# Kernel optimization log

Measured on AMD Instinct MI355X. Metric: run time of the kernel, lower is better.

## Reference

```python
import jax, jax.numpy as jnp
import numpy as np

I, H = 4, 64


def setup_inputs() -> dict:
    key = jax.random.key(0)
    ks = jax.random.split(key, 7)
    s_ih = 1.0 / np.sqrt(H)
    return {
        "x": jax.random.normal(ks[0], (8192, 512, I), dtype=jnp.float32),
        "W_ih": jax.random.uniform(ks[1], (4 * H, I), minval=-s_ih, maxval=s_ih, dtype=jnp.float32),
        "W_hh": jax.random.uniform(ks[2], (4 * H, H), minval=-s_ih, maxval=s_ih, dtype=jnp.float32),
        "b_ih": jax.random.uniform(ks[3], (4 * H,), minval=-s_ih, maxval=s_ih, dtype=jnp.float32),
        "b_hh": jax.random.uniform(ks[4], (4 * H,), minval=-s_ih, maxval=s_ih, dtype=jnp.float32),
        "W_fc": jax.random.uniform(ks[5], (1, H), minval=-s_ih, maxval=s_ih, dtype=jnp.float32),
        "b_fc": jax.random.uniform(ks[6], (1,), minval=-s_ih, maxval=s_ih, dtype=jnp.float32),
    }


def _lstm_last_hidden(x, W_ih, W_hh, b_ih, b_hh):
    # x: [B, T, I] batch_first; PyTorch gate order: i, f, g, o
    B = x.shape[0]
    # Precompute input projections for all timesteps in one GEMM: [T, B, 4H]
    xg = jnp.einsum('bti,gi->tbg', x, W_ih) + (b_ih + b_hh)

    def step(carry, xg_t):
        h, c = carry
        gates = xg_t + h @ W_hh.T  # [B, 4H]
        i, f, g, o = jnp.split(gates, 4, axis=-1)
        i = jax.nn.sigmoid(i)
        f = jax.nn.sigmoid(f)
        g = jnp.tanh(g)
        o = jax.nn.sigmoid(o)
        c = f * c + i * g
        h = o * jnp.tanh(c)
        return (h, c), None

    h0 = jnp.zeros((B, W_hh.shape[1]), dtype=x.dtype)
    c0 = jnp.zeros_like(h0)
    (h_n, _), _ = jax.lax.scan(step, (h0, c0), xg)
    return h_n  # [B, H]


def reference(x, W_ih, W_hh, b_ih, b_hh, W_fc, b_fc):
    h_n = _lstm_last_hidden(x, W_ih, W_hh, b_ih, b_hh)
    return h_n @ W_fc.T + b_fc  # [B, 1]
```

## Files before the change

### kernel.cpp

```cpp
#include <hip/hip_runtime.h>


typedef float f32x4 __attribute__((ext_vector_type(4)));
typedef _Float16 f16x8 __attribute__((ext_vector_type(8)));
typedef _Float16 f16x4 __attribute__((ext_vector_type(4)));

#define TSEQ 512
#define IDIM 4
#define BPB 16
#define TCH 32
#define NCH (TSEQ / TCH)
#define L2E 1.44269504088896340736f

#if __has_builtin(__builtin_amdgcn_exp2f)
#define EX2(v) __builtin_amdgcn_exp2f(v)
#else
#define EX2(v) exp2f(v)
#endif
#define RCP(v) __builtin_amdgcn_rcpf(v)

#define STEP_BARRIER() do {                                   \
    asm volatile("s_waitcnt lgkmcnt(0)" ::: "memory");        \
    __builtin_amdgcn_s_barrier();                             \
    __builtin_amdgcn_sched_barrier(0);                        \
} while (0)

__global__ __launch_bounds__(256, 2) void lstm_fused(
    const float* __restrict__ x,
    const float* __restrict__ W_ih,
    const float* __restrict__ W_hh,
    const float* __restrict__ b_ih,
    const float* __restrict__ b_hh,
    const float* __restrict__ W_fc,
    const float* __restrict__ b_fc,
    float* __restrict__ out)
{
    __shared__ __align__(16) _Float16 hbuf[2][BPB * 64];
    __shared__ __align__(16) f16x4    xstage[2][BPB][33];

    const int tid  = threadIdx.x;
    const int lane = tid & 63;
    const int wv   = tid >> 6;
    const int b0   = blockIdx.x * BPB;
    const int r    = lane & 15;
    const int g16  = lane >> 4;

    f16x8 bfrag[4][3];
    #pragma unroll
    for (int t4 = 0; t4 < 4; ++t4) {
        const float sc = (t4 == 2) ? 2.0f * L2E : L2E;
        const int g = t4 * 64 + wv * 16 + r;
        #pragma unroll
        for (int ks = 0; ks < 2; ++ks) {
            const float* p = W_hh + g * 64 + ks * 32 + g16 * 8;
            f16x8 f;
            #pragma unroll
            for (int j = 0; j < 8; ++j) f[j] = (_Float16)(p[j] * sc);
            bfrag[t4][ks] = f;
        }
        f16x8 f;
        #pragma unroll
        for (int j = 0; j < 8; ++j) f[j] = (_Float16)0.0f;
        if (g16 == 0) {
            #pragma unroll
            for (int j = 0; j < 4; ++j) f[j] = (_Float16)(W_ih[g * IDIM + j] * sc);
            float biasf = (b_ih[g] + b_hh[g]) * sc;
            _Float16 hi = (_Float16)biasf;
            f[4] = hi;
            f[5] = (_Float16)(biasf - (float)hi);
        }
        bfrag[t4][2] = f;
    }
    const float wfc = W_fc[lane];
    const float bfc = b_fc[0];
    const f32x4 zero4 = {0.f, 0.f, 0.f, 0.f};

    float c_reg[4] = {0.f, 0.f, 0.f, 0.f};
    for (int i = tid; i < BPB * 64; i += 256) hbuf[0][i] = (_Float16)0.0f;

    const int bb0 = tid >> 5, tf = tid & 31;
    const float* xg0 = x + ((size_t)(b0 + bb0)     * TSEQ + tf) * IDIM;
    const float* xg1 = x + ((size_t)(b0 + bb0 + 8) * TSEQ + tf) * IDIM;
    float4 xn0 = *(const float4*)xg0;
    float4 xn1 = *(const float4*)xg1;
    {
        f16x4 s0, s1;
        s0[0] = (_Float16)xn0.x; s0[1] = (_Float16)xn0.y;
        s0[2] = (_Float16)xn0.z; s0[3] = (_Float16)xn0.w;
        s1[0] = (_Float16)xn1.x; s1[1] = (_Float16)xn1.y;
        s1[2] = (_Float16)xn1.z; s1[3] = (_Float16)xn1.w;
        xstage[0][bb0][tf]     = s0;
        xstage[0][bb0 + 8][tf] = s1;
    }
    __syncthreads();
    xn0 = *(const float4*)(xg0 + TCH * IDIM);
    xn1 = *(const float4*)(xg1 + TCH * IDIM);

    const int hbase = r * 128;
    const int hs0 = ((g16 + 0) << 4) ^ ((r & 7) << 4);
    const int hs1 = ((g16 + 4) << 4) ^ ((r & 7) << 4);
    int hw[4];
    #pragma unroll
    for (int q = 0; q < 4; ++q) {
        const int bat = 4 * g16 + q;
        hw[q] = (bat * 128 + (wv * 16 + r) * 2) ^ ((bat & 7) << 4);
    }
    char* hbB = (char*)&hbuf[0][0];
    const char* xsB = (const char*)&xstage[0][0][0];
    const int xrow = r * 33 * 8;

    f16x8 axr;
    axr[4] = (_Float16)1.0f; axr[5] = (_Float16)1.0f;
    axr[6] = (_Float16)0.0f; axr[7] = (_Float16)0.0f;

    f32x4 accX[4];
    {
        f16x4 xv = *(const f16x4*)(xsB + xrow);
        axr[0] = xv[0]; axr[1] = xv[1]; axr[2] = xv[2]; axr[3] = xv[3];
        #pragma unroll
        for (int t4 = 0; t4 < 4; ++t4)
            accX[t4] = __builtin_amdgcn_mfma_f32_16x16x32_f16(axr, bfrag[t4][2], zero4, 0, 0, 0);
    }

    auto substep = [&](int t, int P) {
        const char* rb = hbB + P * 2048;
        char*       wb = hbB + (P ^ 1) * 2048;
        f16x8 a0 = *(const f16x8*)(rb + hbase + hs0);
        f16x8 a1 = *(const f16x8*)(rb + hbase + hs1);

        f32x4 acc2[4];
        __builtin_amdgcn_s_setprio(1);
        #pragma unroll
        for (int t4 = 0; t4 < 4; ++t4) {
            f32x4 a;
            a = __builtin_amdgcn_mfma_f32_16x16x32_f16(a0, bfrag[t4][0], accX[t4], 0, 0, 0);
            a = __builtin_amdgcn_mfma_f32_16x16x32_f16(a1, bfrag[t4][1], a, 0, 0, 0);
            acc2[t4] = a;
        }
        __builtin_amdgcn_s_setprio(0);

        {
            const int tb = t + 1;
            f16x4 xv = *(const f16x4*)(xsB + ((tb >> 5) & 1) * 4224 + xrow + (tb & 31) * 8);
            axr[0] = xv[0]; axr[1] = xv[1]; axr[2] = xv[2]; axr[3] = xv[3];
            __builtin_amdgcn_s_setprio(1);
            #pragma unroll
            for (int t4 = 0; t4 < 4; ++t4)
                accX[t4] = __builtin_amdgcn_mfma_f32_16x16x32_f16(axr, bfrag[t4][2], zero4, 0, 0, 0);
            __builtin_amdgcn_s_setprio(0);
        }

        #pragma unroll
        for (int q = 0; q < 4; ++q) {
            float ei = EX2(-acc2[0][q]);
            float ef = EX2(-acc2[1][q]);
            float eg = EX2(-acc2[2][q]);
            float eo = EX2(-acc2[3][q]);
            float A  = 1.f + ei, F = 1.f + ef;
            float Gp = 1.f + eg, Gm = 1.f - eg;
            float P2  = A * Gp;
            float num = c_reg[q] * P2 + Gm * F;
            float c   = num * RCP(P2 * F);
            c_reg[q] = c;
            float uc = fminf(fmaxf(c * (2.0f * L2E), -60.f), 60.f);
            float et = EX2(-uc);
            float h  = (1.f - et) * RCP((1.f + eo) * (1.f + et));
            *(_Float16*)(wb + hw[q]) = (_Float16)h;
        }
        STEP_BARRIER();
    };

    for (int t = 0; t < TSEQ; t += 2) {
        if ((t & (TCH - 1)) == 16) {
            const int c = t >> 5;
            if (c + 1 < NCH) {
                f16x4 s0, s1;
                s0[0] = (_Float16)xn0.x; s0[1] = (_Float16)xn0.y;
                s0[2] = (_Float16)xn0.z; s0[3] = (_Float16)xn0.w;
                s1[0] = (_Float16)xn1.x; s1[1] = (_Float16)xn1.y;
                s1[2] = (_Float16)xn1.z; s1[3] = (_Float16)xn1.w;
                f16x4* dst = &xstage[(c + 1) & 1][0][0];
                dst[bb0 * 33 + tf]       = s0;
                dst[(bb0 + 8) * 33 + tf] = s1;
                if (c + 2 < NCH) {
                    xn0 = *(const float4*)(xg0 + (size_t)(c + 2) * TCH * IDIM);
                    xn1 = *(const float4*)(xg1 + (size_t)(c + 2) * TCH * IDIM);
                }
            }
        }
        substep(t,     0);
        substep(t + 1, 1);
    }

    #pragma unroll
    for (int q = 0; q < 4; ++q) {
        const int bat  = wv * 4 + q;
        const int byte = (bat * 128 + lane * 2) ^ ((bat & 7) << 4);
        float hv = (float)*(const _Float16*)(hbB + byte);
        float partial = hv * wfc;
        #pragma unroll
        for (int off = 32; off > 0; off >>= 1)
            partial += __shfl_down(partial, off);
        if (lane == 0) out[b0 + bat] = partial + bfc;
    }
}

extern "C" void kernel_launch(void* const* d_in, const int* in_sizes, int n_in,
                              void* d_out, int out_size, void* d_ws, size_t ws_size,
                              hipStream_t stream) {
    const float* x    = (const float*)d_in[0];
    const float* W_ih = (const float*)d_in[1];
    const float* W_hh = (const float*)d_in[2];
    const float* b_ih = (const float*)d_in[3];
    const float* b_hh = (const float*)d_in[4];
    const float* W_fc = (const float*)d_in[5];
    const float* b_fc = (const float*)d_in[6];
    float* out = (float*)d_out;

    const int B = in_sizes[0] / (TSEQ * IDIM);
    lstm_fused<<<B / BPB, 256, 0, stream>>>(x, W_ih, W_hh, b_ih, b_hh, W_fc, b_fc, out);
}
```

Before: 338.7 us.

## Inline input-projection MFMA into recurrent chain and stagger alternate blocks

Removes the software-pipelined precomputation of the input projection for the next step and instead chains a third MFMA (x·W_ih plus bias) after the two recurrent MFMAs, starting from zero. It also drops the sched_barrier from the step barrier so the compiler can reorder across steps. Odd blocks (by a simple blockIdx hash) sleep briefly at start to desynchronise co-resident blocks so their MFMA and transcendental phases interleave. The cost is a longer dependent MFMA chain on the critical path per step.

```diff
diff --git a/kernel.cpp b/kernel.cpp
--- a/kernel.cpp
+++ b/kernel.cpp
@@ -22,7 +22,6 @@
 #define STEP_BARRIER() do {                                   \
     asm volatile("s_waitcnt lgkmcnt(0)" ::: "memory");        \
     __builtin_amdgcn_s_barrier();                             \
-    __builtin_amdgcn_sched_barrier(0);                        \
 } while (0)
 
 __global__ __launch_bounds__(256, 2) void lstm_fused(
@@ -96,6 +95,9 @@
     xn0 = *(const float4*)(xg0 + TCH * IDIM);
     xn1 = *(const float4*)(xg1 + TCH * IDIM);
 
+    if (((blockIdx.x ^ (blockIdx.x >> 8)) & 1) != 0)
+        __builtin_amdgcn_s_sleep(13);
+
     const int hbase = r * 128;
     const int hs0 = ((g16 + 0) << 4) ^ ((r & 7) << 4);
     const int hs1 = ((g16 + 4) << 4) ^ ((r & 7) << 4);
@@ -109,53 +111,35 @@
     const char* xsB = (const char*)&xstage[0][0][0];
     const int xrow = r * 33 * 8;
 
-    f16x8 axr;
-    axr[4] = (_Float16)1.0f; axr[5] = (_Float16)1.0f;
-    axr[6] = (_Float16)0.0f; axr[7] = (_Float16)0.0f;
-
-    f32x4 accX[4];
-    {
-        f16x4 xv = *(const f16x4*)(xsB + xrow);
-        axr[0] = xv[0]; axr[1] = xv[1]; axr[2] = xv[2]; axr[3] = xv[3];
-        #pragma unroll
-        for (int t4 = 0; t4 < 4; ++t4)
-            accX[t4] = __builtin_amdgcn_mfma_f32_16x16x32_f16(axr, bfrag[t4][2], zero4, 0, 0, 0);
-    }
-
     auto substep = [&](int t, int P) {
         const char* rb = hbB + P * 2048;
         char*       wb = hbB + (P ^ 1) * 2048;
         f16x8 a0 = *(const f16x8*)(rb + hbase + hs0);
         f16x8 a1 = *(const f16x8*)(rb + hbase + hs1);
-
-        f32x4 acc2[4];
+        f16x4 xv = *(const f16x4*)(xsB + ((t >> 5) & 1) * 4224 + xrow + (t & 31) * 8);
+        f16x8 ax;
+        ax[0] = xv[0]; ax[1] = xv[1]; ax[2] = xv[2]; ax[3] = xv[3];
+        ax[4] = (_Float16)1.0f; ax[5] = (_Float16)1.0f;
+        ax[6] = (_Float16)0.0f; ax[7] = (_Float16)0.0f;
+
+        f32x4 acc[4];
         __builtin_amdgcn_s_setprio(1);
         #pragma unroll
         for (int t4 = 0; t4 < 4; ++t4) {
             f32x4 a;
-            a = __builtin_amdgcn_mfma_f32_16x16x32_f16(a0, bfrag[t4][0], accX[t4], 0, 0, 0);
+            a = __builtin_amdgcn_mfma_f32_16x16x32_f16(a0, bfrag[t4][0], zero4, 0, 0, 0);
             a = __builtin_amdgcn_mfma_f32_16x16x32_f16(a1, bfrag[t4][1], a, 0, 0, 0);
-            acc2[t4] = a;
+            a = __builtin_amdgcn_mfma_f32_16x16x32_f16(ax, bfrag[t4][2], a, 0, 0, 0);
+            acc[t4] = a;
         }
         __builtin_amdgcn_s_setprio(0);
 
-        {
-            const int tb = t + 1;
-            f16x4 xv = *(const f16x4*)(xsB + ((tb >> 5) & 1) * 4224 + xrow + (tb & 31) * 8);
-            axr[0] = xv[0]; axr[1] = xv[1]; axr[2] = xv[2]; axr[3] = xv[3];
-            __builtin_amdgcn_s_setprio(1);
-            #pragma unroll
-            for (int t4 = 0; t4 < 4; ++t4)
-                accX[t4] = __builtin_amdgcn_mfma_f32_16x16x32_f16(axr, bfrag[t4][2], zero4, 0, 0, 0);
-            __builtin_amdgcn_s_setprio(0);
-        }
-
         #pragma unroll
         for (int q = 0; q < 4; ++q) {
-            float ei = EX2(-acc2[0][q]);
-            float ef = EX2(-acc2[1][q]);
-            float eg = EX2(-acc2[2][q]);
-            float eo = EX2(-acc2[3][q]);
+            float ei = EX2(-acc[0][q]);
+            float ef = EX2(-acc[1][q]);
+            float eg = EX2(-acc[2][q]);
+            float eo = EX2(-acc[3][q]);
             float A  = 1.f + ei, F = 1.f + ef;
             float Gp = 1.f + eg, Gm = 1.f - eg;
             float P2  = A * Gp;
```

Result: faster. 323.9 us (-4.4%).
